# Optimization experiments

Measured on AMD Instinct MI355X. Metric: run time of the kernel, lower is better.

The kernel has to match this reference:

```python
import jax, jax.numpy as jnp
import numpy as np

IMG = 224                      # hardcoded image_size in apply_mask
K = int(0.25 * IMG * IMG)      # 12544 pixels masked per sample


def setup_inputs() -> dict:
    key = jax.random.key(0)
    k1, k2 = jax.random.split(key)
    B = 256
    data = jax.random.normal(k1, (B, IMG, IMG, 3), dtype=jnp.float32)
    # |gradients| flattened over (H, W, C) -> length IMG*IMG*3, nonnegative
    line_grad = jax.random.uniform(k2, (B, IMG * IMG * 3), dtype=jnp.float32)
    return {"data": data, "line_grad": line_grad}


def _mask_one(d, g):
    # d: [IMG, IMG, 3], g: [IMG*IMG*3]
    _, idx = jax.lax.top_k(g, K)              # flat indices into (H,W,C)
    reduced = jnp.mod(idx, IMG * IMG)         # fold channel offset -> spatial
    rows = reduced // IMG
    cols = reduced % IMG
    # scatter zeros across all 3 channels at the selected pixels
    return d.at[rows, cols].set(0.0)


def reference(data, line_grad):
    # vectorized_map over the batch -> vmap
    return jax.vmap(_mask_one)(data, line_grad)
```

## Files before the change

### kernel.cpp

```cpp
#include <hip/hip_runtime.h>

#define IMG    224
#define NPIX   (IMG * IMG)
#define NELEM  (NPIX * 3)
#define KSEL   12544
#define NBINS  4096
#define MAXCAND 1024
#define BLOCK  1024
#define NWAVE  (BLOCK / 64)
#define SPLIT  2
#define NPIX4  (NPIX / 4)
#define GVEC   (NELEM / 4)
#define HGVEC  (GVEC / SPLIT)
#define PGRP   (NPIX4 / SPLIT)

typedef float f4 __attribute__((ext_vector_type(4)));

__device__ __forceinline__ int binof(float x) {
    return min((int)(x * 4096.0f), NBINS - 1);
}

__global__ __launch_bounds__(BLOCK) void k1_hist(
    const float* __restrict__ grad, unsigned int* __restrict__ hist)
{
    const int smp  = blockIdx.x / SPLIT;
    const int half = blockIdx.x % SPLIT;
    const int tid  = threadIdx.x;

    __shared__ unsigned int lh[NBINS];
    for (int i = tid; i < NBINS; i += BLOCK) lh[i] = 0u;
    __syncthreads();

    const f4* g4 = (const f4*)(grad + (size_t)smp * NELEM) + (size_t)half * HGVEC;

    int i = tid;
    for (; i + 3 * BLOCK < HGVEC; i += 4 * BLOCK) {
        f4 v0 = g4[i];
        f4 v1 = g4[i + BLOCK];
        f4 v2 = g4[i + 2 * BLOCK];
        f4 v3 = g4[i + 3 * BLOCK];
        #pragma unroll
        for (int c = 0; c < 4; ++c) atomicAdd(&lh[binof(v0[c])], 1u);
        #pragma unroll
        for (int c = 0; c < 4; ++c) atomicAdd(&lh[binof(v1[c])], 1u);
        #pragma unroll
        for (int c = 0; c < 4; ++c) atomicAdd(&lh[binof(v2[c])], 1u);
        #pragma unroll
        for (int c = 0; c < 4; ++c) atomicAdd(&lh[binof(v3[c])], 1u);
    }
    for (; i < HGVEC; i += BLOCK) {
        f4 v = g4[i];
        #pragma unroll
        for (int c = 0; c < 4; ++c) atomicAdd(&lh[binof(v[c])], 1u);
    }
    __syncthreads();

    unsigned int* h = hist + (size_t)smp * NBINS;
    for (int i2 = tid; i2 < NBINS; i2 += BLOCK) atomicAdd(&h[i2], lh[i2]);
}

__global__ __launch_bounds__(BLOCK) void k2_thresh(
    const unsigned int* __restrict__ hist,
    int* __restrict__ B1a, unsigned int* __restrict__ Ra)
{
    const int smp  = blockIdx.x;
    const int tid  = threadIdx.x;
    const int lane = tid & 63;
    const int wid  = tid >> 6;

    __shared__ unsigned int wtot[NWAVE];

    uint4 h = ((const uint4*)(hist + (size_t)smp * NBINS))[tid];
    unsigned int s = h.x + h.y + h.z + h.w;

    unsigned int v = s;
    #pragma unroll
    for (int off = 1; off < 64; off <<= 1) {
        unsigned int u = __shfl_down(v, off);
        if (lane + off < 64) v += u;
    }
    if (lane == 0) wtot[wid] = v;
    __syncthreads();

    unsigned int woff = 0;
    for (int w = wid + 1; w < NWAVE; ++w) woff += wtot[w];

    unsigned int a  = v + woff;
    unsigned int nx = a - s;

    if (a >= KSEL && nx < KSEL) {
        unsigned int hh[4] = {h.x, h.y, h.z, h.w};
        unsigned int cum = nx;
        for (int i = 3; i >= 0; --i) {
            cum += hh[i];
            if (cum >= KSEL) {
                B1a[smp] = 4 * tid + i;
                Ra[smp]  = KSEL - (cum - hh[i]);
                break;
            }
        }
    }
}

__global__ __launch_bounds__(BLOCK) void k3_out(
    const float* __restrict__ data, const float* __restrict__ grad,
    float* __restrict__ out,
    const int* __restrict__ B1a,
    unsigned int* __restrict__ candcnt,
    unsigned int* __restrict__ candkey, unsigned int* __restrict__ candidx)
{
    const int smp  = blockIdx.x / SPLIT;
    const int half = blockIdx.x % SPLIT;
    const int tid  = threadIdx.x;
    const int B1   = B1a[smp];

    const f4* g4 = (const f4*)(grad + (size_t)smp * NELEM);
    const f4* d4 = (const f4*)(data + (size_t)smp * NELEM);
    f4*       o4 = (f4*)(out + (size_t)smp * NELEM);

    unsigned int* ck = candkey + (size_t)smp * MAXCAND;
    unsigned int* ci = candidx + (size_t)smp * MAXCAND;

    auto push = [&](float val, unsigned int idx) {
        unsigned int c2 = atomicAdd(&candcnt[smp], 1u);
        if (c2 < MAXCAND) {
            ck[c2] = __float_as_uint(val);
            ci[c2] = idx;
        }
    };

    for (int q = tid; q < PGRP; q += BLOCK) {
        const int G = half * PGRP + q;
        f4 pa = g4[G];
        f4 pb = g4[G + NPIX4];
        f4 pc = g4[G + 2 * NPIX4];
        f4 x0 = __builtin_nontemporal_load(&d4[3 * G]);
        f4 x1 = __builtin_nontemporal_load(&d4[3 * G + 1]);
        f4 x2 = __builtin_nontemporal_load(&d4[3 * G + 2]);

        bool m[4];
        #pragma unroll
        for (int j = 0; j < 4; ++j) {
            int ba = binof(pa[j]);
            int bb = binof(pb[j]);
            int bc = binof(pc[j]);
            m[j] = (ba > B1) || (bb > B1) || (bc > B1);
            unsigned int p = (unsigned int)(4 * G + j);
            if (ba == B1) push(pa[j], p);
            if (bb == B1) push(pb[j], p + NPIX);
            if (bc == B1) push(pc[j], p + 2 * NPIX);
        }

        if (m[0]) { x0.x = 0.0f; x0.y = 0.0f; x0.z = 0.0f; }
        if (m[1]) { x0.w = 0.0f; x1.x = 0.0f; x1.y = 0.0f; }
        if (m[2]) { x1.z = 0.0f; x1.w = 0.0f; x2.x = 0.0f; }
        if (m[3]) { x2.y = 0.0f; x2.z = 0.0f; x2.w = 0.0f; }

        __builtin_nontemporal_store(x0, &o4[3 * G]);
        __builtin_nontemporal_store(x1, &o4[3 * G + 1]);
        __builtin_nontemporal_store(x2, &o4[3 * G + 2]);
    }
}

__global__ __launch_bounds__(256) void k4_fix(
    float* __restrict__ out,
    const unsigned int* __restrict__ candcnt,
    const unsigned int* __restrict__ candkey,
    const unsigned int* __restrict__ candidx,
    const unsigned int* __restrict__ Ra)
{
    const int smp = blockIdx.x;
    const int t   = threadIdx.x;

    __shared__ unsigned int sk[MAXCAND];
    __shared__ unsigned int si[MAXCAND];

    unsigned int n = candcnt[smp];
    if (n > MAXCAND) n = MAXCAND;
    unsigned int r = Ra[smp];

    const unsigned int* ck = candkey + (size_t)smp * MAXCAND;
    const unsigned int* ci = candidx + (size_t)smp * MAXCAND;
    for (unsigned int j = t; j < n; j += 256) { sk[j] = ck[j]; si[j] = ci[j]; }
    __syncthreads();

    for (unsigned int j = t; j < n; j += 256) {
        unsigned int kj = sk[j];
        unsigned int ij = si[j];
        unsigned int rank = 0;
        for (unsigned int i = 0; i < n; ++i) {
            unsigned int ki = sk[i];
            rank += (ki > kj) || (ki == kj && si[i] < ij);
        }
        if (rank < r) {
            unsigned int p = ij % NPIX;
            float* op = out + (size_t)smp * NELEM + 3u * p;
            op[0] = 0.0f; op[1] = 0.0f; op[2] = 0.0f;
        }
    }
}

__global__ __launch_bounds__(BLOCK) void masked_model_kernel(
    const float* __restrict__ data,
    const float* __restrict__ grad,
    float* __restrict__ out)
{
    const int b    = blockIdx.x;
    const int tid  = threadIdx.x;
    const int lane = tid & 63;
    const int wid  = tid >> 6;

    const float* g = grad + (size_t)b * NELEM;
    const float* d = data + (size_t)b * NELEM;
    float*       o = out  + (size_t)b * NELEM;

    __shared__ unsigned int hist[NBINS];
    __shared__ unsigned int mask[NPIX / 32];
    __shared__ unsigned int candkey[MAXCAND];
    __shared__ unsigned int candidx[MAXCAND];
    __shared__ unsigned int wtot[NWAVE];
    __shared__ unsigned int candcnt;
    __shared__ int sB1;
    __shared__ unsigned int sR;

    for (int i = tid; i < NBINS; i += BLOCK) hist[i] = 0u;
    for (int i = tid; i < NPIX / 32; i += BLOCK) mask[i] = 0u;
    if (tid == 0) candcnt = 0u;
    __syncthreads();

    const f4* g4 = (const f4*)g;
    for (int i = tid; i < GVEC; i += BLOCK) {
        f4 v = g4[i];
        #pragma unroll
        for (int c = 0; c < 4; ++c) atomicAdd(&hist[binof(v[c])], 1u);
    }
    __syncthreads();

    {
        unsigned int s = hist[4 * tid] + hist[4 * tid + 1]
                       + hist[4 * tid + 2] + hist[4 * tid + 3];
        unsigned int v = s;
        #pragma unroll
        for (int off = 1; off < 64; off <<= 1) {
            unsigned int u = __shfl_down(v, off);
            if (lane + off < 64) v += u;
        }
        if (lane == 0) wtot[wid] = v;
        __syncthreads();
        unsigned int woff = 0;
        for (int w = wid + 1; w < NWAVE; ++w) woff += wtot[w];
        unsigned int a  = v + woff;
        unsigned int nx = a - s;
        if (a >= KSEL && nx < KSEL) {
            unsigned int cum = nx;
            for (int i = 3; i >= 0; --i) {
                unsigned int h = hist[4 * tid + i];
                cum += h;
                if (cum >= KSEL) { sB1 = 4 * tid + i; sR = KSEL - (cum - h); break; }
            }
        }
    }
    __syncthreads();

    {
        const int B1 = sB1;
        for (int i = tid; i < GVEC; i += BLOCK) {
            f4 v = g4[i];
            #pragma unroll
            for (int c = 0; c < 4; ++c) {
                int bin = binof(v[c]);
                int idx = 4 * i + c;
                if (bin > B1) {
                    int p = idx % NPIX;
                    atomicOr(&mask[p >> 5], 1u << (p & 31));
                } else if (bin == B1) {
                    unsigned int c2 = atomicAdd(&candcnt, 1u);
                    if (c2 < MAXCAND) {
                        candkey[c2] = __float_as_uint(v[c]);
                        candidx[c2] = (unsigned int)idx;
                    }
                }
            }
        }
    }
    __syncthreads();

    {
        unsigned int n = candcnt < MAXCAND ? candcnt : MAXCAND;
        unsigned int r = sR;
        for (unsigned int j = tid; j < n; j += BLOCK) {
            unsigned int kj = candkey[j];
            unsigned int ij = candidx[j];
            unsigned int rank = 0;
            for (unsigned int i = 0; i < n; ++i) {
                unsigned int ki = candkey[i];
                rank += (ki > kj) || (ki == kj && candidx[i] < ij);
            }
            if (rank < r) {
                int p = (int)(ij % NPIX);
                atomicOr(&mask[p >> 5], 1u << (p & 31));
            }
        }
    }
    __syncthreads();

    {
        const f4* d4 = (const f4*)d;
        f4*       o4 = (f4*)o;
        for (int i = tid; i < GVEC; i += BLOCK) {
            f4 v = d4[i];
            int e = 4 * i;
            int p0 = e / 3, p1 = (e + 1) / 3, p2 = (e + 2) / 3, p3 = (e + 3) / 3;
            if ((mask[p0 >> 5] >> (p0 & 31)) & 1u) v.x = 0.0f;
            if ((mask[p1 >> 5] >> (p1 & 31)) & 1u) v.y = 0.0f;
            if ((mask[p2 >> 5] >> (p2 & 31)) & 1u) v.z = 0.0f;
            if ((mask[p3 >> 5] >> (p3 & 31)) & 1u) v.w = 0.0f;
            o4[i] = v;
        }
    }
}

extern "C" void kernel_launch(void* const* d_in, const int* in_sizes, int n_in,
                              void* d_out, int out_size, void* d_ws, size_t ws_size,
                              hipStream_t stream) {
    const float* data = (const float*)d_in[0];
    const float* grad = (const float*)d_in[1];
    float* out = (float*)d_out;

    const int B = in_sizes[0] / NELEM;

    const size_t histB  = (size_t)B * NBINS * 4;
    const size_t cntB   = (size_t)B * 4;
    const size_t candB  = (size_t)B * MAXCAND * 4;
    const size_t needed = histB + 3 * cntB + 2 * candB;

    if (ws_size < needed) {
        masked_model_kernel<<<B, BLOCK, 0, stream>>>(data, grad, out);
        return;
    }

    char* ws = (char*)d_ws;
    unsigned int* hist    = (unsigned int*)(ws);
    unsigned int* candcnt = (unsigned int*)(ws + histB);
    int*          B1a     = (int*)         (ws + histB + cntB);
    unsigned int* Ra      = (unsigned int*)(ws + histB + 2 * cntB);
    unsigned int* candkey = (unsigned int*)(ws + histB + 3 * cntB);
    unsigned int* candidx = (unsigned int*)(ws + histB + 3 * cntB + candB);

    hipMemsetAsync(ws, 0, histB + cntB, stream);

    k1_hist  <<<B * SPLIT, BLOCK, 0, stream>>>(grad, hist);
    k2_thresh<<<B,         BLOCK, 0, stream>>>(hist, B1a, Ra);
    k3_out   <<<B * SPLIT, BLOCK, 0, stream>>>(data, grad, out, B1a, candcnt, candkey, candidx);
    k4_fix   <<<B,         256,   0, stream>>>(out, candcnt, candkey, candidx, Ra);
}
```

Measured before the change: 404.1 us.

## Fuse top-k mask pipeline into one cooperative kernel with grid syncs

Replaces the memset plus four-kernel launch sequence with a single cooperative kernel that builds per-half histograms, exchanges them through global memory across a grid sync, computes the threshold locally, classifies and copies, then does the boundary-bin rank fix after a second grid sync. Classification now writes a shared-memory bitmask via wave ballots, and the data copy becomes a contiguous streaming pass instead of per-pixel three-vector loads. The aim is to remove launch gaps, the memset and global histogram atomics. The cost is that the 512 blocks of 1024 threads must all be co-resident, and the grid syncs add barrier latency. If the cooperative launch fails, it falls back to the split kernels.

```diff
diff --git a/kernel.cpp b/kernel.cpp
--- a/kernel.cpp
+++ b/kernel.cpp
@@ -1,4 +1,7 @@
 #include <hip/hip_runtime.h>
+#include <hip/hip_cooperative_groups.h>
+
+namespace cg = cooperative_groups;
 
 #define IMG    224
 #define NPIX   (IMG * IMG)
@@ -13,6 +16,8 @@
 #define GVEC   (NELEM / 4)
 #define HGVEC  (GVEC / SPLIT)
 #define PGRP   (NPIX4 / SPLIT)
+#define NMWH   (NPIX / SPLIT / 32)
+#define EVH    (3 * PGRP)
 
 typedef float f4 __attribute__((ext_vector_type(4)));
 
@@ -20,25 +25,23 @@
     return min((int)(x * 4096.0f), NBINS - 1);
 }
 
-__global__ __launch_bounds__(BLOCK) void k1_hist(
-    const float* __restrict__ grad, unsigned int* __restrict__ hist)
-{
-    const int smp  = blockIdx.x / SPLIT;
-    const int half = blockIdx.x % SPLIT;
-    const int tid  = threadIdx.x;
-
-    __shared__ unsigned int lh[NBINS];
-    for (int i = tid; i < NBINS; i += BLOCK) lh[i] = 0u;
-    __syncthreads();
-
-    const f4* g4 = (const f4*)(grad + (size_t)smp * NELEM) + (size_t)half * HGVEC;
-
+__device__ __forceinline__ unsigned int spread4(unsigned int x) {
+    x = (x | (x << 12)) & 0x000F000Fu;
+    x = (x | (x << 6))  & 0x03030303u;
+    x = (x | (x << 3))  & 0x11111111u;
+    return x;
+}
+
+
+__device__ __forceinline__ void hist_accum(const f4* __restrict__ g4h,
+                                           unsigned int* lh, int tid)
+{
     int i = tid;
     for (; i + 3 * BLOCK < HGVEC; i += 4 * BLOCK) {
-        f4 v0 = g4[i];
-        f4 v1 = g4[i + BLOCK];
-        f4 v2 = g4[i + 2 * BLOCK];
-        f4 v3 = g4[i + 3 * BLOCK];
+        f4 v0 = g4h[i];
+        f4 v1 = g4h[i + BLOCK];
+        f4 v2 = g4h[i + 2 * BLOCK];
+        f4 v3 = g4h[i + 3 * BLOCK];
         #pragma unroll
         for (int c = 0; c < 4; ++c) atomicAdd(&lh[binof(v0[c])], 1u);
         #pragma unroll
@@ -49,30 +52,19 @@
         for (int c = 0; c < 4; ++c) atomicAdd(&lh[binof(v3[c])], 1u);
     }
     for (; i < HGVEC; i += BLOCK) {
-        f4 v = g4[i];
+        f4 v = g4h[i];
         #pragma unroll
         for (int c = 0; c < 4; ++c) atomicAdd(&lh[binof(v[c])], 1u);
     }
-    __syncthreads();
-
-    unsigned int* h = hist + (size_t)smp * NBINS;
-    for (int i2 = tid; i2 < NBINS; i2 += BLOCK) atomicAdd(&h[i2], lh[i2]);
-}
-
-__global__ __launch_bounds__(BLOCK) void k2_thresh(
-    const unsigned int* __restrict__ hist,
-    int* __restrict__ B1a, unsigned int* __restrict__ Ra)
-{
-    const int smp  = blockIdx.x;
-    const int tid  = threadIdx.x;
+}
+
+__device__ __forceinline__ void threshold_scan(
+    unsigned int h0, unsigned int h1, unsigned int h2, unsigned int h3,
+    unsigned int* wtot, int* sB1, unsigned int* sR, int tid)
+{
     const int lane = tid & 63;
     const int wid  = tid >> 6;
-
-    __shared__ unsigned int wtot[NWAVE];
-
-    uint4 h = ((const uint4*)(hist + (size_t)smp * NBINS))[tid];
-    unsigned int s = h.x + h.y + h.z + h.w;
-
+    unsigned int s = h0 + h1 + h2 + h3;
     unsigned int v = s;
     #pragma unroll
     for (int off = 1; off < 64; off <<= 1) {
@@ -81,110 +73,118 @@
     }
     if (lane == 0) wtot[wid] = v;
     __syncthreads();
-
     unsigned int woff = 0;
     for (int w = wid + 1; w < NWAVE; ++w) woff += wtot[w];
-
     unsigned int a  = v + woff;
     unsigned int nx = a - s;
-
     if (a >= KSEL && nx < KSEL) {
-        unsigned int hh[4] = {h.x, h.y, h.z, h.w};
+        unsigned int hh[4] = {h0, h1, h2, h3};
         unsigned int cum = nx;
         for (int i = 3; i >= 0; --i) {
             cum += hh[i];
             if (cum >= KSEL) {
-                B1a[smp] = 4 * tid + i;
-                Ra[smp]  = KSEL - (cum - hh[i]);
+                *sB1 = 4 * tid + i;
+                *sR  = KSEL - (cum - hh[i]);
                 break;
             }
         }
     }
-}
-
-__global__ __launch_bounds__(BLOCK) void k3_out(
-    const float* __restrict__ data, const float* __restrict__ grad,
-    float* __restrict__ out,
-    const int* __restrict__ B1a,
-    unsigned int* __restrict__ candcnt,
-    unsigned int* __restrict__ candkey, unsigned int* __restrict__ candidx)
-{
-    const int smp  = blockIdx.x / SPLIT;
-    const int half = blockIdx.x % SPLIT;
-    const int tid  = threadIdx.x;
-    const int B1   = B1a[smp];
-
-    const f4* g4 = (const f4*)(grad + (size_t)smp * NELEM);
-    const f4* d4 = (const f4*)(data + (size_t)smp * NELEM);
-    f4*       o4 = (f4*)(out + (size_t)smp * NELEM);
-
-    unsigned int* ck = candkey + (size_t)smp * MAXCAND;
-    unsigned int* ci = candidx + (size_t)smp * MAXCAND;
+    __syncthreads();
+}
+
+__device__ __forceinline__ void classify_copy(
+    const f4* __restrict__ g4, const f4* __restrict__ d4, f4* __restrict__ o4,
+    int half, int B1, unsigned int* maskw,
+    unsigned int* cnt, unsigned int* ck, unsigned int* ci, int tid)
+{
+    const int lane = tid & 63;
+    const int wid  = tid >> 6;
 
     auto push = [&](float val, unsigned int idx) {
-        unsigned int c2 = atomicAdd(&candcnt[smp], 1u);
+        unsigned int c2 = atomicAdd(cnt, 1u);
         if (c2 < MAXCAND) {
             ck[c2] = __float_as_uint(val);
             ci[c2] = idx;
         }
     };
 
-    for (int q = tid; q < PGRP; q += BLOCK) {
-        const int G = half * PGRP + q;
-        f4 pa = g4[G];
-        f4 pb = g4[G + NPIX4];
-        f4 pc = g4[G + 2 * NPIX4];
-        f4 x0 = __builtin_nontemporal_load(&d4[3 * G]);
-        f4 x1 = __builtin_nontemporal_load(&d4[3 * G + 1]);
-        f4 x2 = __builtin_nontemporal_load(&d4[3 * G + 2]);
-
+    for (int q0 = 0; q0 < PGRP; q0 += BLOCK) {
+        const int q   = q0 + tid;
+        const bool inb = q < PGRP;
+        const int G   = half * PGRP + q;
+        f4 pa = {0.f, 0.f, 0.f, 0.f}, pb = pa, pc = pa;
+        if (inb) {
+            pa = g4[G];
+            pb = g4[G + NPIX4];
+            pc = g4[G + 2 * NPIX4];
+        }
         bool m[4];
         #pragma unroll
         for (int j = 0; j < 4; ++j) {
             int ba = binof(pa[j]);
             int bb = binof(pb[j]);
             int bc = binof(pc[j]);
-            m[j] = (ba > B1) || (bb > B1) || (bc > B1);
+            m[j] = inb && ((ba > B1) || (bb > B1) || (bc > B1));
             unsigned int p = (unsigned int)(4 * G + j);
-            if (ba == B1) push(pa[j], p);
-            if (bb == B1) push(pb[j], p + NPIX);
-            if (bc == B1) push(pc[j], p + 2 * NPIX);
-        }
-
-        if (m[0]) { x0.x = 0.0f; x0.y = 0.0f; x0.z = 0.0f; }
-        if (m[1]) { x0.w = 0.0f; x1.x = 0.0f; x1.y = 0.0f; }
-        if (m[2]) { x1.z = 0.0f; x1.w = 0.0f; x2.x = 0.0f; }
-        if (m[3]) { x2.y = 0.0f; x2.z = 0.0f; x2.w = 0.0f; }
-
-        __builtin_nontemporal_store(x0, &o4[3 * G]);
-        __builtin_nontemporal_store(x1, &o4[3 * G + 1]);
-        __builtin_nontemporal_store(x2, &o4[3 * G + 2]);
-    }
-}
-
-__global__ __launch_bounds__(256) void k4_fix(
-    float* __restrict__ out,
-    const unsigned int* __restrict__ candcnt,
-    const unsigned int* __restrict__ candkey,
-    const unsigned int* __restrict__ candidx,
-    const unsigned int* __restrict__ Ra)
-{
-    const int smp = blockIdx.x;
-    const int t   = threadIdx.x;
-
-    __shared__ unsigned int sk[MAXCAND];
-    __shared__ unsigned int si[MAXCAND];
-
-    unsigned int n = candcnt[smp];
-    if (n > MAXCAND) n = MAXCAND;
-    unsigned int r = Ra[smp];
-
-    const unsigned int* ck = candkey + (size_t)smp * MAXCAND;
-    const unsigned int* ci = candidx + (size_t)smp * MAXCAND;
-    for (unsigned int j = t; j < n; j += 256) { sk[j] = ck[j]; si[j] = ci[j]; }
-    __syncthreads();
-
-    for (unsigned int j = t; j < n; j += 256) {
+            if (inb && ba == B1) push(pa[j], p);
+            if (inb && bb == B1) push(pb[j], p + NPIX);
+            if (inb && bc == B1) push(pc[j], p + 2 * NPIX);
+        }
+        unsigned long long bl[4];
+        #pragma unroll
+        for (int j = 0; j < 4; ++j) bl[j] = __ballot(m[j]);
+
+        const int qb = q0 + wid * 64;
+        if (lane < 8 && qb < PGRP) {
+            unsigned int w =
+                  spread4((unsigned int)(bl[0] >> (8 * lane)) & 0xFFu)
+                | (spread4((unsigned int)(bl[1] >> (8 * lane)) & 0xFFu) << 1)
+                | (spread4((unsigned int)(bl[2] >> (8 * lane)) & 0xFFu) << 2)
+                | (spread4((unsigned int)(bl[3] >> (8 * lane)) & 0xFFu) << 3);
+            maskw[(qb >> 3) + lane] = w;
+        }
+    }
+    __syncthreads();
+
+    const f4* dh = d4 + (size_t)half * EVH;
+    f4*       oh = o4 + (size_t)half * EVH;
+    auto msk = [&](int lp) -> unsigned int {
+        return (maskw[lp >> 5] >> (lp & 31)) & 1u;
+    };
+    auto app = [&](f4 v, int i) -> f4 {
+        int x = 4 * i;
+        int p0 = x / 3, p1 = (x + 1) / 3, p2 = (x + 2) / 3, p3 = (x + 3) / 3;
+        if (msk(p0)) v.x = 0.0f;
+        if (msk(p1)) v.y = 0.0f;
+        if (msk(p2)) v.z = 0.0f;
+        if (msk(p3)) v.w = 0.0f;
+        return v;
+    };
+    int i = tid;
+    for (; i + 3 * BLOCK < EVH; i += 4 * BLOCK) {
+        f4 v0 = __builtin_nontemporal_load(&dh[i]);
+        f4 v1 = __builtin_nontemporal_load(&dh[i + BLOCK]);
+        f4 v2 = __builtin_nontemporal_load(&dh[i + 2 * BLOCK]);
+        f4 v3 = __builtin_nontemporal_load(&dh[i + 3 * BLOCK]);
+        __builtin_nontemporal_store(app(v0, i),             &oh[i]);
+        __builtin_nontemporal_store(app(v1, i + BLOCK),     &oh[i + BLOCK]);
+        __builtin_nontemporal_store(app(v2, i + 2 * BLOCK), &oh[i + 2 * BLOCK]);
+        __builtin_nontemporal_store(app(v3, i + 3 * BLOCK), &oh[i + 3 * BLOCK]);
+    }
+    for (; i < EVH; i += BLOCK) {
+        f4 v = __builtin_nontemporal_load(&dh[i]);
+        __builtin_nontemporal_store(app(v, i), &oh[i]);
+    }
+}
+
+__device__ __forceinline__ void rank_fix(
+    float* __restrict__ o, const unsigned int* __restrict__ ck,
+    const unsigned int* __restrict__ ci, unsigned int n, unsigned int r,
+    unsigned int* sk, unsigned int* si, int tid, int nthreads)
+{
+    for (unsigned int j = tid; j < n; j += nthreads) { sk[j] = ck[j]; si[j] = ci[j]; }
+    __syncthreads();
+    for (unsigned int j = tid; j < n; j += nthreads) {
         unsigned int kj = sk[j];
         unsigned int ij = si[j];
         unsigned int rank = 0;
@@ -194,10 +194,163 @@
         }
         if (rank < r) {
             unsigned int p = ij % NPIX;
-            float* op = out + (size_t)smp * NELEM + 3u * p;
+            float* op = o + 3u * p;
             op[0] = 0.0f; op[1] = 0.0f; op[2] = 0.0f;
         }
     }
+}
+
+__global__ __launch_bounds__(BLOCK, 8) void fused_all(
+    const float* __restrict__ data, const float* __restrict__ grad,
+    float* __restrict__ out, unsigned int* __restrict__ hist2,
+    unsigned int* __restrict__ candcnt,
+    unsigned int* __restrict__ candkey, unsigned int* __restrict__ candidx)
+{
+    const int smp  = blockIdx.x / SPLIT;
+    const int half = blockIdx.x % SPLIT;
+    const int tid  = threadIdx.x;
+
+    __shared__ unsigned int lh[NBINS];
+    __shared__ unsigned int maskw[NMWH];
+    __shared__ unsigned int wtot[NWAVE];
+    __shared__ int sB1;
+    __shared__ unsigned int sR;
+    __shared__ unsigned int sk[MAXCAND];
+    __shared__ unsigned int si[MAXCAND];
+
+    for (int i = tid; i < NBINS; i += BLOCK) lh[i] = 0u;
+    if (tid == 0 && half == 0) candcnt[smp] = 0u;
+    __syncthreads();
+
+    const f4* g4 = (const f4*)(grad + (size_t)smp * NELEM);
+
+    hist_accum(g4 + (size_t)half * HGVEC, lh, tid);
+    __syncthreads();
+
+    {
+        uint4* dst = (uint4*)(hist2 + ((size_t)smp * SPLIT + half) * NBINS);
+        uint4 v;
+        v.x = lh[4 * tid]; v.y = lh[4 * tid + 1];
+        v.z = lh[4 * tid + 2]; v.w = lh[4 * tid + 3];
+        dst[tid] = v;
+    }
+
+    cg::this_grid().sync();
+
+    {
+        const unsigned int* hoth = hist2 + ((size_t)smp * SPLIT + (half ^ 1)) * NBINS;
+        uint4 ho = ((const uint4*)hoth)[tid];
+        threshold_scan(lh[4 * tid] + ho.x, lh[4 * tid + 1] + ho.y,
+                       lh[4 * tid + 2] + ho.z, lh[4 * tid + 3] + ho.w,
+                       wtot, &sB1, &sR, tid);
+    }
+
+    const f4* d4 = (const f4*)(data + (size_t)smp * NELEM);
+    f4*       o4 = (f4*)(out + (size_t)smp * NELEM);
+    classify_copy(g4, d4, o4, half, sB1, maskw,
+                  candcnt + smp,
+                  candkey + (size_t)smp * MAXCAND,
+                  candidx + (size_t)smp * MAXCAND, tid);
+
+    cg::this_grid().sync();
+
+    if (half == 0) {
+        unsigned int n = candcnt[smp];
+        if (n > MAXCAND) n = MAXCAND;
+        rank_fix(out + (size_t)smp * NELEM,
+                 candkey + (size_t)smp * MAXCAND,
+                 candidx + (size_t)smp * MAXCAND,
+                 n, sR, sk, si, tid, BLOCK);
+    }
+}
+
+__global__ __launch_bounds__(BLOCK, 8) void k1_hist(
+    const float* __restrict__ grad, unsigned int* __restrict__ hist2)
+{
+    const int smp  = blockIdx.x / SPLIT;
+    const int half = blockIdx.x % SPLIT;
+    const int tid  = threadIdx.x;
+
+    __shared__ unsigned int lh[NBINS];
+    for (int i = tid; i < NBINS; i += BLOCK) lh[i] = 0u;
+    __syncthreads();
+
+    const f4* g4 = (const f4*)(grad + (size_t)smp * NELEM) + (size_t)half * HGVEC;
+    hist_accum(g4, lh, tid);
+    __syncthreads();
+
+    uint4* dst = (uint4*)(hist2 + ((size_t)smp * SPLIT + half) * NBINS);
+    uint4 v;
+    v.x = lh[4 * tid]; v.y = lh[4 * tid + 1];
+    v.z = lh[4 * tid + 2]; v.w = lh[4 * tid + 3];
+    dst[tid] = v;
+}
+
+__global__ __launch_bounds__(BLOCK) void k2_thresh(
+    const unsigned int* __restrict__ hist2,
+    int* __restrict__ B1a, unsigned int* __restrict__ Ra,
+    unsigned int* __restrict__ candcnt)
+{
+    const int smp = blockIdx.x;
+    const int tid = threadIdx.x;
+
+    __shared__ unsigned int wtot[NWAVE];
+    __shared__ int sB1;
+    __shared__ unsigned int sR;
+
+    uint4 h0 = ((const uint4*)(hist2 + ((size_t)smp * SPLIT)     * NBINS))[tid];
+    uint4 h1 = ((const uint4*)(hist2 + ((size_t)smp * SPLIT + 1) * NBINS))[tid];
+    threshold_scan(h0.x + h1.x, h0.y + h1.y, h0.z + h1.z, h0.w + h1.w,
+                   wtot, &sB1, &sR, tid);
+
+    if (tid == 0) {
+        B1a[smp] = sB1;
+        Ra[smp]  = sR;
+        candcnt[smp] = 0u;
+    }
+}
+
+__global__ __launch_bounds__(BLOCK, 8) void k3_out(
+    const float* __restrict__ data, const float* __restrict__ grad,
+    float* __restrict__ out, const int* __restrict__ B1a,
+    unsigned int* __restrict__ candcnt,
+    unsigned int* __restrict__ candkey, unsigned int* __restrict__ candidx)
+{
+    const int smp  = blockIdx.x / SPLIT;
+    const int half = blockIdx.x % SPLIT;
+    const int tid  = threadIdx.x;
+
+    __shared__ unsigned int maskw[NMWH];
+
+    const f4* g4 = (const f4*)(grad + (size_t)smp * NELEM);
+    const f4* d4 = (const f4*)(data + (size_t)smp * NELEM);
+    f4*       o4 = (f4*)(out + (size_t)smp * NELEM);
+
+    classify_copy(g4, d4, o4, half, B1a[smp], maskw,
+                  candcnt + smp,
+                  candkey + (size_t)smp * MAXCAND,
+                  candidx + (size_t)smp * MAXCAND, tid);
+}
+
+__global__ __launch_bounds__(BLOCK) void k4_fix(
+    float* __restrict__ out,
+    const unsigned int* __restrict__ candcnt,
+    const unsigned int* __restrict__ candkey,
+    const unsigned int* __restrict__ candidx,
+    const unsigned int* __restrict__ Ra)
+{
+    const int smp = blockIdx.x;
+    const int tid = threadIdx.x;
+
+    __shared__ unsigned int sk[MAXCAND];
+    __shared__ unsigned int si[MAXCAND];
+
+    unsigned int n = candcnt[smp];
+    if (n > MAXCAND) n = MAXCAND;
+    rank_fix(out + (size_t)smp * NELEM,
+             candkey + (size_t)smp * MAXCAND,
+             candidx + (size_t)smp * MAXCAND,
+             n, Ra[smp], sk, si, tid, BLOCK);
 }
 
 __global__ __launch_bounds__(BLOCK) void masked_model_kernel(
@@ -329,7 +482,7 @@
 
     const int B = in_sizes[0] / NELEM;
 
-    const size_t histB  = (size_t)B * NBINS * 4;
+    const size_t histB  = (size_t)B * SPLIT * NBINS * 4;
     const size_t cntB   = (size_t)B * 4;
     const size_t candB  = (size_t)B * MAXCAND * 4;
     const size_t needed = histB + 3 * cntB + 2 * candB;
@@ -340,17 +493,25 @@
     }
 
     char* ws = (char*)d_ws;
-    unsigned int* hist    = (unsigned int*)(ws);
+    unsigned int* hist2   = (unsigned int*)(ws);
     unsigned int* candcnt = (unsigned int*)(ws + histB);
     int*          B1a     = (int*)         (ws + histB + cntB);
     unsigned int* Ra      = (unsigned int*)(ws + histB + 2 * cntB);
     unsigned int* candkey = (unsigned int*)(ws + histB + 3 * cntB);
     unsigned int* candidx = (unsigned int*)(ws + histB + 3 * cntB + candB);
 
-    hipMemsetAsync(ws, 0, histB + cntB, stream);
-
-    k1_hist  <<<B * SPLIT, BLOCK, 0, stream>>>(grad, hist);
-    k2_thresh<<<B,         BLOCK, 0, stream>>>(hist, B1a, Ra);
-    k3_out   <<<B * SPLIT, BLOCK, 0, stream>>>(data, grad, out, B1a, candcnt, candkey, candidx);
-    k4_fix   <<<B,         256,   0, stream>>>(out, candcnt, candkey, candidx, Ra);
-}
+    void* args[] = { (void*)&data, (void*)&grad, (void*)&out, (void*)&hist2,
+                     (void*)&candcnt, (void*)&candkey, (void*)&candidx };
+    hipError_t e = hipLaunchCooperativeKernel((const void*)fused_all,
+                                              dim3(B * SPLIT), dim3(BLOCK),
+                                              args, 0, stream);
+    if (e != hipSuccess) {
+        (void)hipGetLastError();
+        k1_hist  <<<B * SPLIT, BLOCK, 0, stream>>>(grad, hist2);
+        k2_thresh<<<B,         BLOCK, 0, stream>>>(hist2, B1a, Ra, candcnt);
+        k3_out   <<<B * SPLIT, BLOCK, 0, stream>>>(data, grad, out, B1a,
+                                                   candcnt, candkey, candidx);
+        k4_fix   <<<B,         BLOCK, 0, stream>>>(out, candcnt, candkey,
+                                                   candidx, Ra);
+    }
+}
```

New measurement: 505.6 us. 25.1% more time.
